# Optimization experiments

Measured on AMD Instinct MI355X. Metric: run time of the kernel, lower is better.

The kernel has to match this reference:

```python
import jax, jax.numpy as jnp
import numpy as np

N_NODES = 100000
N_EDGES = 1600000
N_GRAPHS = 1000
NODES_PER_GRAPH = N_NODES // N_GRAPHS
IN_DIM, HID_DIM, OUT_DIM = 32, 64, 32


def setup_inputs() -> dict:
    key = jax.random.key(0)
    k_x, k_src, k_dst, k_w1, k_w2 = jax.random.split(key, 5)
    x = jax.random.normal(k_x, (N_NODES, IN_DIM), dtype=jnp.float32)
    src = jax.random.randint(k_src, (N_EDGES,), 0, N_NODES, dtype=jnp.int32)
    dst = jax.random.randint(k_dst, (N_EDGES,), 0, N_NODES, dtype=jnp.int32)
    edge_index = jnp.stack([src, dst], axis=0)
    batch = (jnp.arange(N_NODES, dtype=jnp.int32) // NODES_PER_GRAPH)
    W1 = jax.random.normal(k_w1, (IN_DIM, HID_DIM), dtype=jnp.float32) / np.sqrt(IN_DIM)
    b1 = jnp.zeros((HID_DIM,), dtype=jnp.float32)
    W2 = jax.random.normal(k_w2, (HID_DIM, OUT_DIM), dtype=jnp.float32) / np.sqrt(HID_DIM)
    b2 = jnp.zeros((OUT_DIM,), dtype=jnp.float32)
    return {"x": x, "edge_index": edge_index, "batch": batch,
            "W1": W1, "b1": b1, "W2": W2, "b2": b2}


def _gcn_conv(x, W, b, src, dst, deg_inv_sqrt):
    # PyG GCNConv: out = D^{-1/2}(A+I)D^{-1/2} X W + b, deg includes self-loops
    h = x @ W  # [N, F]
    norm = deg_inv_sqrt[src] * deg_inv_sqrt[dst]  # [E]
    agg = jax.ops.segment_sum(h[src] * norm[:, None], dst, num_segments=N_NODES)
    # self-loop contribution: norm = deg^{-1/2} * deg^{-1/2} = 1/deg
    agg = agg + h * (deg_inv_sqrt * deg_inv_sqrt)[:, None]
    return agg + b


def reference(x, edge_index, batch, W1, b1, W2, b2):
    src, dst = edge_index[0], edge_index[1]
    # degree at target nodes, with self-loops
    deg = 1.0 + jax.ops.segment_sum(jnp.ones_like(dst, dtype=x.dtype), dst,
                                    num_segments=N_NODES)
    deg_inv_sqrt = jax.lax.rsqrt(deg)
    h = jax.nn.relu(_gcn_conv(x, W1, b1, src, dst, deg_inv_sqrt))
    h = _gcn_conv(h, W2, b2, src, dst, deg_inv_sqrt)
    # per-graph mean pooling (fused segment mean)
    sums = jax.ops.segment_sum(h, batch, num_segments=N_GRAPHS)
    counts = jax.ops.segment_sum(jnp.ones((h.shape[0],), dtype=h.dtype), batch,
                                 num_segments=N_GRAPHS)
    return sums / counts[:, None]
```

## Files before the change

kernel.cpp:

```cpp
#include <hip/hip_runtime.h>

#define IN_DIM 32
#define HID_DIM 64
#define OUT_DIM 32

#define BSHIFT 7
#define BNODES 128
#define BMASK 127
#define MAXBUCK 1024
#define CAP 2560
#define EPB 2048

typedef unsigned int u32;
typedef unsigned short u16;
typedef __attribute__((ext_vector_type(8))) short bf16x8;
typedef __attribute__((ext_vector_type(4))) float f32x4;

static __device__ __forceinline__ u32 bf16rne(float f) {
    u32 u = __float_as_uint(f);
    return (u + 0x7FFFu + ((u >> 16) & 1u)) >> 16;
}
static __device__ __forceinline__ float blo(u32 u) { return __uint_as_float(u << 16); }
static __device__ __forceinline__ float bhi(u32 u) { return __uint_as_float(u & 0xFFFF0000u); }

__global__ __launch_bounds__(256) void k_bin(const int* __restrict__ src,
                                             const int* __restrict__ dst,
                                             int* __restrict__ cursor,
                                             int* __restrict__ binned,
                                             int E, int nbuck) {
    __shared__ int lcnt[MAXBUCK];
    __shared__ int lbase[MAXBUCK];
    int t = threadIdx.x;
#pragma unroll
    for (int k = 0; k < MAXBUCK / 256; k++) lcnt[t + k * 256] = 0;
    __syncthreads();
    int base = blockIdx.x * EPB;
    int dreg[8];
#pragma unroll
    for (int k = 0; k < 8; k++) {
        int e = base + k * 256 + t;
        dreg[k] = (e < E) ? dst[e] : -1;
    }
#pragma unroll
    for (int k = 0; k < 8; k++)
        if (dreg[k] >= 0) atomicAdd(&lcnt[dreg[k] >> BSHIFT], 1);
    __syncthreads();
    for (int b = t; b < nbuck; b += 256) {
        int c = lcnt[b];
        if (c) lbase[b] = atomicAdd(&cursor[b], c);
        lcnt[b] = 0;
    }
    __syncthreads();
#pragma unroll
    for (int k = 0; k < 8; k++) {
        int e = base + k * 256 + t;
        if (dreg[k] >= 0) {
            int d = dreg[k];
            int bk = d >> BSHIFT;
            int loc = lbase[bk] + atomicAdd(&lcnt[bk], 1);
            if (loc < CAP)
                binned[bk * CAP + loc] = ((d & BMASK) << 17) | src[e];
        }
    }
}

__global__ __launch_bounds__(256) void k_csr(const int* __restrict__ binned,
                                             const int* __restrict__ cursor,
                                             const float* __restrict__ x,
                                             int2* __restrict__ row,
                                             float* __restrict__ dis,
                                             u16* __restrict__ g,
                                             int* __restrict__ meta, int N) {
    __shared__ int sEdge[CAP];
    __shared__ int sH[4][BNODES];
    __shared__ int sExcl[BNODES];
    __shared__ int sCur[BNODES];
    __shared__ float sdis[BNODES];
    __shared__ int wsum[2];
    int b = blockIdx.x;
    int t = threadIdx.x;
    int wid = t >> 6;
    int s0 = b * CAP;
    int cnt = cursor[b];
    if (cnt > CAP) cnt = CAP;

    for (int k = t; k < 4 * BNODES; k += 256) ((int*)sH)[k] = 0;
    __syncthreads();

    for (int k = t; k < cnt; k += 256) {
        int p = binned[s0 + k];
        sEdge[k] = p;
        atomicAdd(&sH[wid][p >> 17], 1);
    }
    __syncthreads();

    int myv = 0;
    if (t < BNODES) {
        myv = sH[0][t] + sH[1][t] + sH[2][t] + sH[3][t];
        int lane = t & 63;
        int incl = myv;
#pragma unroll
        for (int o = 1; o < 64; o <<= 1) {
            int up = __shfl_up(incl, o);
            if (lane >= o) incl += up;
        }
        if (lane == 63) wsum[t >> 6] = incl;
        sExcl[t] = incl - myv;
        sCur[t] = 0;
    }
    __syncthreads();
    if (t < BNODES) {
        int exclv = sExcl[t] + ((t >= 64) ? wsum[0] : 0);
        sExcl[t] = exclv;
        float d = rsqrtf(1.0f + (float)myv);
        sdis[t] = d;
        int node = (b << BSHIFT) + t;
        if (node < N) {
            row[node] = make_int2(s0 + exclv, s0 + exclv + myv);
            dis[node] = d;
        }
    }
    __syncthreads();

    for (int k = t; k < cnt; k += 256) {
        int p = sEdge[k];
        int dl = p >> 17;
        int pos = sExcl[dl] + atomicAdd(&sCur[dl], 1);
        meta[s0 + pos] = p & 0x1FFFF;
    }

    int nbLo = b << BSHIFT;
    int nn = N - nbLo;
    if (nn > BNODES) nn = BNODES;
    if (nn < 0) nn = 0;
    int halfE = nn * 16;
    const float* xb = x + (size_t)nbLo * 32;
    u32* gb = (u32*)(g + (size_t)nbLo * 32);
    for (int j = t; j < halfE; j += 256) {
        int e0 = j * 2;
        float dd = sdis[e0 >> 5];
        gb[j] = bf16rne(dd * xb[e0]) | (bf16rne(dd * xb[e0 + 1]) << 16);
    }
}

__global__ __launch_bounds__(256) void k_agg(const u16* __restrict__ g,
                                             const int* __restrict__ meta,
                                             const int2* __restrict__ row,
                                             const float* __restrict__ dis,
                                             u16* __restrict__ outf, int N) {
    int gid = blockIdx.x * 256 + threadIdx.x;
    int i = gid >> 5;
    if (i >= N) return;
    int l = threadIdx.x & 31;
    int grp = (l >> 2) & 7;
    int sub = l & 3;
    const uint4* gv = (const uint4*)g;

    float a0 = 0.f, a1 = 0.f, a2 = 0.f, a3 = 0.f;
    float a4 = 0.f, a5 = 0.f, a6 = 0.f, a7 = 0.f;
    int2 rw = row[i];
    int e = rw.x, end = rw.y;
    for (; e + 16 <= end; e += 16) {
        int s0 = meta[e + grp];
        int s1 = meta[e + 8 + grp];
        uint4 v0 = gv[s0 * 4 + sub];
        uint4 v1 = gv[s1 * 4 + sub];
        a0 += blo(v0.x); a1 += bhi(v0.x); a2 += blo(v0.y); a3 += bhi(v0.y);
        a4 += blo(v0.z); a5 += bhi(v0.z); a6 += blo(v0.w); a7 += bhi(v0.w);
        a0 += blo(v1.x); a1 += bhi(v1.x); a2 += blo(v1.y); a3 += bhi(v1.y);
        a4 += blo(v1.z); a5 += bhi(v1.z); a6 += blo(v1.w); a7 += bhi(v1.w);
    }
    if (e + grp < end) {
        uint4 v = gv[meta[e + grp] * 4 + sub];
        a0 += blo(v.x); a1 += bhi(v.x); a2 += blo(v.y); a3 += bhi(v.y);
        a4 += blo(v.z); a5 += bhi(v.z); a6 += blo(v.w); a7 += bhi(v.w);
    }
    if (e + 8 + grp < end) {
        uint4 v = gv[meta[e + 8 + grp] * 4 + sub];
        a0 += blo(v.x); a1 += bhi(v.x); a2 += blo(v.y); a3 += bhi(v.y);
        a4 += blo(v.z); a5 += bhi(v.z); a6 += blo(v.w); a7 += bhi(v.w);
    }
#pragma unroll
    for (int m = 4; m <= 16; m <<= 1) {
        a0 += __shfl_xor(a0, m); a1 += __shfl_xor(a1, m);
        a2 += __shfl_xor(a2, m); a3 += __shfl_xor(a3, m);
        a4 += __shfl_xor(a4, m); a5 += __shfl_xor(a5, m);
        a6 += __shfl_xor(a6, m); a7 += __shfl_xor(a7, m);
    }
    if (grp == 0) {
        uint4 sv = gv[i * 4 + sub];
        float d = dis[i];
        u32 o0 = bf16rne(d * (a0 + blo(sv.x))) | (bf16rne(d * (a1 + bhi(sv.x))) << 16);
        u32 o1 = bf16rne(d * (a2 + blo(sv.y))) | (bf16rne(d * (a3 + bhi(sv.y))) << 16);
        u32 o2 = bf16rne(d * (a4 + blo(sv.z))) | (bf16rne(d * (a5 + bhi(sv.z))) << 16);
        u32 o3 = bf16rne(d * (a6 + blo(sv.w))) | (bf16rne(d * (a7 + bhi(sv.w))) << 16);
        ((uint4*)outf)[i * 4 + sub] = make_uint4(o0, o1, o2, o3);
    }
}

__global__ __launch_bounds__(256) void k_mlp(const u16* __restrict__ aggX,
                                             const float* __restrict__ W1,
                                             const float* __restrict__ b1,
                                             const float* __restrict__ W2,
                                             const float* __restrict__ b2,
                                             const float* __restrict__ dis,
                                             u16* __restrict__ t2,
                                             float* __restrict__ out,
                                             int N, int outElems) {
    __shared__ float sHls[4][16 * 65];
    int t = threadIdx.x;
    int j = blockIdx.x * 256 + t;
    if (j < outElems) out[j] = b2[j & 31];

    int w = t >> 6;
    int L = t & 63;
    int q = L >> 4;
    int col = L & 15;
    int base = blockIdx.x * 64 + w * 16;

    int arow = base + col;
    uint4 av = (arow < N) ? ((const uint4*)aggX)[(size_t)arow * 4 + q]
                          : make_uint4(0, 0, 0, 0);
    bf16x8 afrag = *(bf16x8*)&av;

    bf16x8 b1f[4];
#pragma unroll
    for (int nt = 0; nt < 4; nt++) {
#pragma unroll
        for (int jj = 0; jj < 8; jj++)
            b1f[nt][jj] = (short)bf16rne(W1[(q * 8 + jj) * HID_DIM + nt * 16 + col]);
    }
    bf16x8 b2f[2][2];
#pragma unroll
    for (int ks = 0; ks < 2; ks++)
#pragma unroll
        for (int nt = 0; nt < 2; nt++) {
#pragma unroll
            for (int jj = 0; jj < 8; jj++)
                b2f[ks][nt][jj] =
                    (short)bf16rne(W2[(ks * 32 + q * 8 + jj) * OUT_DIM + nt * 16 + col]);
        }

    float bias = 0.0f;
#pragma unroll
    for (int nt = 0; nt < 4; nt++) {
        bias = b1[nt * 16 + col];
        f32x4 c = {bias, bias, bias, bias};
        c = __builtin_amdgcn_mfma_f32_16x16x32_bf16(afrag, b1f[nt], c, 0, 0, 0);
#pragma unroll
        for (int r = 0; r < 4; r++)
            sHls[w][(q * 4 + r) * 65 + nt * 16 + col] = fmaxf(c[r], 0.0f);
    }
    __syncthreads();

    bf16x8 a2[2];
#pragma unroll
    for (int ks = 0; ks < 2; ks++) {
#pragma unroll
        for (int jj = 0; jj < 8; jj++)
            a2[ks][jj] = (short)bf16rne(sHls[w][col * 65 + ks * 32 + q * 8 + jj]);
    }

    f32x4 C2[2];
#pragma unroll
    for (int nt = 0; nt < 2; nt++) {
        f32x4 c = {0.f, 0.f, 0.f, 0.f};
        c = __builtin_amdgcn_mfma_f32_16x16x32_bf16(a2[0], b2f[0][nt], c, 0, 0, 0);
        c = __builtin_amdgcn_mfma_f32_16x16x32_bf16(a2[1], b2f[1][nt], c, 0, 0, 0);
        C2[nt] = c;
    }

#pragma unroll
    for (int r = 0; r < 4; r++) {
        int node = base + q * 4 + r;
        if (node < N) {
            float dd = dis[node];
            t2[(size_t)node * 32 + col]      = (u16)bf16rne(dd * C2[0][r]);
            t2[(size_t)node * 32 + 16 + col] = (u16)bf16rne(dd * C2[1][r]);
        }
    }
}

__global__ __launch_bounds__(256) void k_agg_pool(const u16* __restrict__ g,
                                                  const int* __restrict__ meta,
                                                  const int2* __restrict__ row,
                                                  const float* __restrict__ dis,
                                                  float* __restrict__ out,
                                                  int N, int npg, float inv_npg) {
    __shared__ float sval[8][32];
    int t = threadIdx.x;
    int hw = t >> 5;
    int base0 = blockIdx.x * 8;
    int i = base0 + hw;
    int l = t & 31;
    int grp = (l >> 2) & 7;
    int sub = l & 3;
    const uint4* gv = (const uint4*)g;

    float a0 = 0.f, a1 = 0.f, a2 = 0.f, a3 = 0.f;
    float a4 = 0.f, a5 = 0.f, a6 = 0.f, a7 = 0.f;
    bool valid = (i < N);
    if (valid) {
        int2 rw = row[i];
        int e = rw.x, end = rw.y;
        for (; e + 16 <= end; e += 16) {
            int s0 = meta[e + grp];
            int s1 = meta[e + 8 + grp];
            uint4 v0 = gv[s0 * 4 + sub];
            uint4 v1 = gv[s1 * 4 + sub];
            a0 += blo(v0.x); a1 += bhi(v0.x); a2 += blo(v0.y); a3 += bhi(v0.y);
            a4 += blo(v0.z); a5 += bhi(v0.z); a6 += blo(v0.w); a7 += bhi(v0.w);
            a0 += blo(v1.x); a1 += bhi(v1.x); a2 += blo(v1.y); a3 += bhi(v1.y);
            a4 += blo(v1.z); a5 += bhi(v1.z); a6 += blo(v1.w); a7 += bhi(v1.w);
        }
        if (e + grp < end) {
            uint4 v = gv[meta[e + grp] * 4 + sub];
            a0 += blo(v.x); a1 += bhi(v.x); a2 += blo(v.y); a3 += bhi(v.y);
            a4 += blo(v.z); a5 += bhi(v.z); a6 += blo(v.w); a7 += bhi(v.w);
        }
        if (e + 8 + grp < end) {
            uint4 v = gv[meta[e + 8 + grp] * 4 + sub];
            a0 += blo(v.x); a1 += bhi(v.x); a2 += blo(v.y); a3 += bhi(v.y);
            a4 += blo(v.z); a5 += bhi(v.z); a6 += blo(v.w); a7 += bhi(v.w);
        }
    }
#pragma unroll
    for (int m = 4; m <= 16; m <<= 1) {
        a0 += __shfl_xor(a0, m); a1 += __shfl_xor(a1, m);
        a2 += __shfl_xor(a2, m); a3 += __shfl_xor(a3, m);
        a4 += __shfl_xor(a4, m); a5 += __shfl_xor(a5, m);
        a6 += __shfl_xor(a6, m); a7 += __shfl_xor(a7, m);
    }
    if (grp == 0) {
        float4 r0 = make_float4(0.f, 0.f, 0.f, 0.f);
        float4 r1 = make_float4(0.f, 0.f, 0.f, 0.f);
        if (valid) {
            uint4 sv = gv[i * 4 + sub];
            float d = dis[i];
            r0.x = d * (a0 + blo(sv.x)); r0.y = d * (a1 + bhi(sv.x));
            r0.z = d * (a2 + blo(sv.y)); r0.w = d * (a3 + bhi(sv.y));
            r1.x = d * (a4 + blo(sv.z)); r1.y = d * (a5 + bhi(sv.z));
            r1.z = d * (a6 + blo(sv.w)); r1.w = d * (a7 + bhi(sv.w));
        }
        float4* sp = (float4*)&sval[hw][0];
        sp[sub * 2 + 0] = r0;
        sp[sub * 2 + 1] = r1;
    }
    __syncthreads();
    if (t < 32) {
        int gfirst = base0 / npg;
        int bound = (gfirst + 1) * npg;
        float acc = 0.0f;
        int curg = gfirst;
#pragma unroll
        for (int h = 0; h < 8; h++) {
            int node = base0 + h;
            if (node >= N) break;
            int gg = (node >= bound) ? gfirst + 1 : gfirst;
            if (gg != curg) {
                atomicAdd(&out[curg * 32 + t], acc * inv_npg);
                acc = 0.0f;
                curg = gg;
            }
            acc += sval[h][t];
        }
        atomicAdd(&out[curg * 32 + t], acc * inv_npg);
    }
}

extern "C" void kernel_launch(void* const* d_in, const int* in_sizes, int n_in,
                              void* d_out, int out_size, void* d_ws, size_t ws_size,
                              hipStream_t stream) {
    const float* x   = (const float*)d_in[0];
    const int* eidx  = (const int*)d_in[1];
    const float* W1  = (const float*)d_in[3];
    const float* b1  = (const float*)d_in[4];
    const float* W2  = (const float*)d_in[5];
    const float* b2  = (const float*)d_in[6];
    float* out       = (float*)d_out;

    const int N = in_sizes[0] / IN_DIM;
    const int E = in_sizes[1] / 2;
    const int G = out_size / OUT_DIM;
    const int npg = N / G;
    const int nbuck = (N + BNODES - 1) >> BSHIFT;
    const int* src = eidx;
    const int* dst = eidx + E;

    char* ws = (char*)d_ws;
    size_t off = 0;
    auto alloc = [&](size_t bytes) -> char* {
        char* p = ws + off;
        off = (off + bytes + 255) & ~(size_t)255;
        return p;
    };
    int*   cursor = (int*)alloc(MAXBUCK * sizeof(int));
    int2*  row    = (int2*)alloc((size_t)N * sizeof(int2));
    float* dis    = (float*)alloc((size_t)N * sizeof(float));
    int*   binned = (int*)alloc((size_t)nbuck * CAP * sizeof(int));
    int*   meta   = (int*)alloc((size_t)nbuck * CAP * sizeof(int));
    u16*   g      = (u16*)alloc((size_t)N * IN_DIM * sizeof(u16));
    u16*   bufA   = (u16*)alloc((size_t)N * IN_DIM * sizeof(u16));
    u16*   bufB   = (u16*)alloc((size_t)N * OUT_DIM * sizeof(u16));
    (void)ws_size;

    hipMemsetAsync(cursor, 0, MAXBUCK * sizeof(int), stream);

    k_bin<<<(E + EPB - 1) / EPB, 256, 0, stream>>>(src, dst, cursor, binned, E, nbuck);
    k_csr<<<nbuck, 256, 0, stream>>>(binned, cursor, x, row, dis, g, meta, N);
    k_agg<<<((size_t)N * 32 + 255) / 256, 256, 0, stream>>>(g, meta, row, dis, bufA, N);
    k_mlp<<<(N + 63) / 64, 256, 0, stream>>>(bufA, W1, b1, W2, b2, dis, bufB, out,
                                             N, G * OUT_DIM);
    k_agg_pool<<<(N + 7) / 8, 256, 0, stream>>>(bufB, meta, row, dis, out,
                                                N, npg, 1.0f / (float)npg);
}
```

Before: 192.6 us.

## Widen binning buckets to 256 nodes and split CSR build across two blocks

The edge binning pass now uses 256-node buckets, halving the bucket count. This means fewer global cursor atomics per binning block and fewer, larger contiguous bins. The CSR-building kernel launches two blocks per bucket. Each block redundantly loads and histograms the whole bucket, then writes row/degree data, meta entries and scaled features only for its own 128-node half. The trade-off is duplicated loading and histogramming of bucket edges in exchange for coarser bins, and CAP per bucket doubles.

```diff
diff --git a/kernel.cpp b/kernel.cpp
--- a/kernel.cpp
+++ b/kernel.cpp
@@ -4,11 +4,10 @@
 #define HID_DIM 64
 #define OUT_DIM 32
 
-#define BSHIFT 7
-#define BNODES 128
-#define BMASK 127
-#define MAXBUCK 1024
-#define CAP 2560
+#define WSHIFT 8
+#define WMASK 255
+#define MAXBUCK 512
+#define CAP 5120
 #define EPB 2048
 
 typedef unsigned int u32;
@@ -31,8 +30,7 @@
     __shared__ int lcnt[MAXBUCK];
     __shared__ int lbase[MAXBUCK];
     int t = threadIdx.x;
-#pragma unroll
-    for (int k = 0; k < MAXBUCK / 256; k++) lcnt[t + k * 256] = 0;
+    lcnt[t] = 0; lcnt[t + 256] = 0;
     __syncthreads();
     int base = blockIdx.x * EPB;
     int dreg[8];
@@ -43,7 +41,7 @@
     }
 #pragma unroll
     for (int k = 0; k < 8; k++)
-        if (dreg[k] >= 0) atomicAdd(&lcnt[dreg[k] >> BSHIFT], 1);
+        if (dreg[k] >= 0) atomicAdd(&lcnt[dreg[k] >> WSHIFT], 1);
     __syncthreads();
     for (int b = t; b < nbuck; b += 256) {
         int c = lcnt[b];
@@ -56,10 +54,10 @@
         int e = base + k * 256 + t;
         if (dreg[k] >= 0) {
             int d = dreg[k];
-            int bk = d >> BSHIFT;
+            int bk = d >> WSHIFT;
             int loc = lbase[bk] + atomicAdd(&lcnt[bk], 1);
             if (loc < CAP)
-                binned[bk * CAP + loc] = ((d & BMASK) << 17) | src[e];
+                binned[bk * CAP + loc] = ((d & WMASK) << 17) | src[e];
         }
     }
 }
@@ -72,19 +70,21 @@
                                              u16* __restrict__ g,
                                              int* __restrict__ meta, int N) {
     __shared__ int sEdge[CAP];
-    __shared__ int sH[4][BNODES];
-    __shared__ int sExcl[BNODES];
-    __shared__ int sCur[BNODES];
-    __shared__ float sdis[BNODES];
-    __shared__ int wsum[2];
-    int b = blockIdx.x;
+    __shared__ int sH[4][256];
+    __shared__ int sExcl[256];
+    __shared__ int sCur[128];
+    __shared__ float sdis[128];
+    __shared__ int wsum[4];
+    int bb = blockIdx.x;
+    int b = bb >> 1;
+    int h = bb & 1;
     int t = threadIdx.x;
     int wid = t >> 6;
     int s0 = b * CAP;
     int cnt = cursor[b];
     if (cnt > CAP) cnt = CAP;
 
-    for (int k = t; k < 4 * BNODES; k += 256) ((int*)sH)[k] = 0;
+    for (int k = t; k < 4 * 256; k += 256) ((int*)sH)[k] = 0;
     __syncthreads();
 
     for (int k = t; k < cnt; k += 256) {
@@ -94,27 +94,29 @@
     }
     __syncthreads();
 
-    int myv = 0;
-    if (t < BNODES) {
-        myv = sH[0][t] + sH[1][t] + sH[2][t] + sH[3][t];
-        int lane = t & 63;
-        int incl = myv;
-#pragma unroll
-        for (int o = 1; o < 64; o <<= 1) {
-            int up = __shfl_up(incl, o);
-            if (lane >= o) incl += up;
-        }
-        if (lane == 63) wsum[t >> 6] = incl;
-        sExcl[t] = incl - myv;
-        sCur[t] = 0;
-    }
-    __syncthreads();
-    if (t < BNODES) {
-        int exclv = sExcl[t] + ((t >= 64) ? wsum[0] : 0);
-        sExcl[t] = exclv;
+    int myv = sH[0][t] + sH[1][t] + sH[2][t] + sH[3][t];
+    int lane = t & 63;
+    int incl = myv;
+#pragma unroll
+    for (int o = 1; o < 64; o <<= 1) {
+        int up = __shfl_up(incl, o);
+        if (lane >= o) incl += up;
+    }
+    if (lane == 63) wsum[wid] = incl;
+    sExcl[t] = incl - myv;
+    if (t < 128) sCur[t] = 0;
+    __syncthreads();
+    int wpre = 0;
+#pragma unroll
+    for (int w = 0; w < 4; w++) wpre += (w < wid) ? wsum[w] : 0;
+    int exclv = sExcl[t] + wpre;
+    sExcl[t] = exclv;
+
+    bool mine = ((t >> 7) == h);
+    if (mine) {
         float d = rsqrtf(1.0f + (float)myv);
-        sdis[t] = d;
-        int node = (b << BSHIFT) + t;
+        sdis[t & 127] = d;
+        int node = (b << WSHIFT) + t;
         if (node < N) {
             row[node] = make_int2(s0 + exclv, s0 + exclv + myv);
             dis[node] = d;
@@ -125,13 +127,15 @@
     for (int k = t; k < cnt; k += 256) {
         int p = sEdge[k];
         int dl = p >> 17;
-        int pos = sExcl[dl] + atomicAdd(&sCur[dl], 1);
-        meta[s0 + pos] = p & 0x1FFFF;
-    }
-
-    int nbLo = b << BSHIFT;
+        if ((dl >> 7) == h) {
+            int pos = sExcl[dl] + atomicAdd(&sCur[dl & 127], 1);
+            meta[s0 + pos] = p & 0x1FFFF;
+        }
+    }
+
+    int nbLo = (b << WSHIFT) + h * 128;
     int nn = N - nbLo;
-    if (nn > BNODES) nn = BNODES;
+    if (nn > 128) nn = 128;
     if (nn < 0) nn = 0;
     int halfE = nn * 16;
     const float* xb = x + (size_t)nbLo * 32;
@@ -241,10 +245,9 @@
                     (short)bf16rne(W2[(ks * 32 + q * 8 + jj) * OUT_DIM + nt * 16 + col]);
         }
 
-    float bias = 0.0f;
 #pragma unroll
     for (int nt = 0; nt < 4; nt++) {
-        bias = b1[nt * 16 + col];
+        float bias = b1[nt * 16 + col];
         f32x4 c = {bias, bias, bias, bias};
         c = __builtin_amdgcn_mfma_f32_16x16x32_bf16(afrag, b1f[nt], c, 0, 0, 0);
 #pragma unroll
@@ -383,7 +386,7 @@
     const int E = in_sizes[1] / 2;
     const int G = out_size / OUT_DIM;
     const int npg = N / G;
-    const int nbuck = (N + BNODES - 1) >> BSHIFT;
+    const int nbuck = (N + 255) >> WSHIFT;
     const int* src = eidx;
     const int* dst = eidx + E;
 
@@ -407,7 +410,7 @@
     hipMemsetAsync(cursor, 0, MAXBUCK * sizeof(int), stream);
 
     k_bin<<<(E + EPB - 1) / EPB, 256, 0, stream>>>(src, dst, cursor, binned, E, nbuck);
-    k_csr<<<nbuck, 256, 0, stream>>>(binned, cursor, x, row, dis, g, meta, N);
+    k_csr<<<2 * nbuck, 256, 0, stream>>>(binned, cursor, x, row, dis, g, meta, N);
     k_agg<<<((size_t)N * 32 + 255) / 256, 256, 0, stream>>>(g, meta, row, dis, bufA, N);
     k_mlp<<<(N + 63) / 64, 256, 0, stream>>>(bufA, W1, b1, W2, b2, dis, bufB, out,
                                              N, G * OUT_DIM);
```

After: 189.5 us. No clear change (-1.6%).

## Bucket edges by graph and pool second layer per graph without per-node aggregation

Applied to the files above, without the earlier changes.

Edges are now bucketed by graph (npg nodes per bucket, via magic-number division) instead of fixed 128-node buckets. The final layer-2 aggregation plus mean pooling is replaced by a per-graph kernel. Because pooling is linear, it sums dis[dst]*g[src] over the edges in each bucket plus the self terms directly, so per-node layer-2 outputs and global float atomics are never formed. This removes the CSR walk over all nodes in the last layer and moves bias initialisation into the pool kernel. In exchange, one 256-thread block handles each graph's roughly 1600 edges. The change also assumes npg is at most 128 and that nodes are contiguously batched.

```diff
diff --git a/kernel.cpp b/kernel.cpp
--- a/kernel.cpp
+++ b/kernel.cpp
@@ -4,15 +4,13 @@
 #define HID_DIM 64
 #define OUT_DIM 32
 
-#define BSHIFT 7
-#define BNODES 128
-#define BMASK 127
 #define MAXBUCK 1024
 #define CAP 2560
 #define EPB 2048
 
 typedef unsigned int u32;
 typedef unsigned short u16;
+typedef unsigned long long u64;
 typedef __attribute__((ext_vector_type(8))) short bf16x8;
 typedef __attribute__((ext_vector_type(4))) float f32x4;
 
@@ -27,7 +25,7 @@
                                              const int* __restrict__ dst,
                                              int* __restrict__ cursor,
                                              int* __restrict__ binned,
-                                             int E, int nbuck) {
+                                             int E, int nbuck, int npg, u32 M) {
     __shared__ int lcnt[MAXBUCK];
     __shared__ int lbase[MAXBUCK];
     int t = threadIdx.x;
@@ -35,15 +33,19 @@
     for (int k = 0; k < MAXBUCK / 256; k++) lcnt[t + k * 256] = 0;
     __syncthreads();
     int base = blockIdx.x * EPB;
-    int dreg[8];
+    int dreg[8], breg[8];
 #pragma unroll
     for (int k = 0; k < 8; k++) {
         int e = base + k * 256 + t;
         dreg[k] = (e < E) ? dst[e] : -1;
     }
 #pragma unroll
-    for (int k = 0; k < 8; k++)
-        if (dreg[k] >= 0) atomicAdd(&lcnt[dreg[k] >> BSHIFT], 1);
+    for (int k = 0; k < 8; k++) {
+        if (dreg[k] >= 0) {
+            breg[k] = (int)(((u64)(u32)dreg[k] * M) >> 38);
+            atomicAdd(&lcnt[breg[k]], 1);
+        }
+    }
     __syncthreads();
     for (int b = t; b < nbuck; b += 256) {
         int c = lcnt[b];
@@ -53,13 +55,12 @@
     __syncthreads();
 #pragma unroll
     for (int k = 0; k < 8; k++) {
-        int e = base + k * 256 + t;
         if (dreg[k] >= 0) {
-            int d = dreg[k];
-            int bk = d >> BSHIFT;
+            int bk = breg[k];
+            int dl = dreg[k] - bk * npg;
             int loc = lbase[bk] + atomicAdd(&lcnt[bk], 1);
             if (loc < CAP)
-                binned[bk * CAP + loc] = ((d & BMASK) << 17) | src[e];
+                binned[bk * CAP + loc] = (dl << 17) | src[base + k * 256 + t];
         }
     }
 }
@@ -70,12 +71,13 @@
                                              int2* __restrict__ row,
                                              float* __restrict__ dis,
                                              u16* __restrict__ g,
-                                             int* __restrict__ meta, int N) {
+                                             int* __restrict__ meta,
+                                             int N, int npg) {
     __shared__ int sEdge[CAP];
-    __shared__ int sH[4][BNODES];
-    __shared__ int sExcl[BNODES];
-    __shared__ int sCur[BNODES];
-    __shared__ float sdis[BNODES];
+    __shared__ int sH[4][128];
+    __shared__ int sExcl[128];
+    __shared__ int sCur[128];
+    __shared__ float sdis[128];
     __shared__ int wsum[2];
     int b = blockIdx.x;
     int t = threadIdx.x;
@@ -84,7 +86,7 @@
     int cnt = cursor[b];
     if (cnt > CAP) cnt = CAP;
 
-    for (int k = t; k < 4 * BNODES; k += 256) ((int*)sH)[k] = 0;
+    for (int k = t; k < 4 * 128; k += 256) ((int*)sH)[k] = 0;
     __syncthreads();
 
     for (int k = t; k < cnt; k += 256) {
@@ -94,9 +96,8 @@
     }
     __syncthreads();
 
-    int myv = 0;
-    if (t < BNODES) {
-        myv = sH[0][t] + sH[1][t] + sH[2][t] + sH[3][t];
+    if (t < 128) {
+        int myv = sH[0][t] + sH[1][t] + sH[2][t] + sH[3][t];
         int lane = t & 63;
         int incl = myv;
 #pragma unroll
@@ -107,15 +108,17 @@
         if (lane == 63) wsum[t >> 6] = incl;
         sExcl[t] = incl - myv;
         sCur[t] = 0;
-    }
-    __syncthreads();
-    if (t < BNODES) {
+        sH[0][t] = myv;
+    }
+    __syncthreads();
+    if (t < 128) {
         int exclv = sExcl[t] + ((t >= 64) ? wsum[0] : 0);
         sExcl[t] = exclv;
+        int myv = sH[0][t];
         float d = rsqrtf(1.0f + (float)myv);
         sdis[t] = d;
-        int node = (b << BSHIFT) + t;
-        if (node < N) {
+        int node = b * npg + t;
+        if (t < npg && node < N) {
             row[node] = make_int2(s0 + exclv, s0 + exclv + myv);
             dis[node] = d;
         }
@@ -129,9 +132,9 @@
         meta[s0 + pos] = p & 0x1FFFF;
     }
 
-    int nbLo = b << BSHIFT;
+    int nbLo = b * npg;
     int nn = N - nbLo;
-    if (nn > BNODES) nn = BNODES;
+    if (nn > npg) nn = npg;
     if (nn < 0) nn = 0;
     int halfE = nn * 16;
     const float* xb = x + (size_t)nbLo * 32;
@@ -202,16 +205,10 @@
                                              const float* __restrict__ W1,
                                              const float* __restrict__ b1,
                                              const float* __restrict__ W2,
-                                             const float* __restrict__ b2,
                                              const float* __restrict__ dis,
-                                             u16* __restrict__ t2,
-                                             float* __restrict__ out,
-                                             int N, int outElems) {
+                                             u16* __restrict__ t2, int N) {
     __shared__ float sHls[4][16 * 65];
     int t = threadIdx.x;
-    int j = blockIdx.x * 256 + t;
-    if (j < outElems) out[j] = b2[j & 31];
-
     int w = t >> 6;
     int L = t & 63;
     int q = L >> 4;
@@ -241,10 +238,9 @@
                     (short)bf16rne(W2[(ks * 32 + q * 8 + jj) * OUT_DIM + nt * 16 + col]);
         }
 
-    float bias = 0.0f;
 #pragma unroll
     for (int nt = 0; nt < 4; nt++) {
-        bias = b1[nt * 16 + col];
+        float bias = b1[nt * 16 + col];
         f32x4 c = {bias, bias, bias, bias};
         c = __builtin_amdgcn_mfma_f32_16x16x32_bf16(afrag, b1f[nt], c, 0, 0, 0);
 #pragma unroll
@@ -281,91 +277,87 @@
     }
 }
 
-__global__ __launch_bounds__(256) void k_agg_pool(const u16* __restrict__ g,
-                                                  const int* __restrict__ meta,
-                                                  const int2* __restrict__ row,
-                                                  const float* __restrict__ dis,
-                                                  float* __restrict__ out,
-                                                  int N, int npg, float inv_npg) {
-    __shared__ float sval[8][32];
+__global__ __launch_bounds__(256) void k_pool2(const int* __restrict__ binned,
+                                               const int* __restrict__ cursor,
+                                               const u16* __restrict__ gB,
+                                               const float* __restrict__ dis,
+                                               const float* __restrict__ b2,
+                                               float* __restrict__ out,
+                                               int N, int npg, float inv_npg) {
+    __shared__ float sdis[128];
+    __shared__ float sacc[32];
+    int b = blockIdx.x;
     int t = threadIdx.x;
-    int hw = t >> 5;
-    int base0 = blockIdx.x * 8;
-    int i = base0 + hw;
-    int l = t & 31;
-    int grp = (l >> 2) & 7;
-    int sub = l & 3;
-    const uint4* gv = (const uint4*)g;
+    if (t < 128) {
+        int node = b * npg + t;
+        sdis[t] = (t < npg && node < N) ? dis[node] : 0.0f;
+    }
+    if (t < 32) sacc[t] = 0.0f;
+    __syncthreads();
+
+    int s0 = b * CAP;
+    int cnt = cursor[b];
+    if (cnt > CAP) cnt = CAP;
+    int sub = t & 3;
+    int et = t >> 2;
+    const uint4* gv = (const uint4*)gB;
 
     float a0 = 0.f, a1 = 0.f, a2 = 0.f, a3 = 0.f;
     float a4 = 0.f, a5 = 0.f, a6 = 0.f, a7 = 0.f;
-    bool valid = (i < N);
-    if (valid) {
-        int2 rw = row[i];
-        int e = rw.x, end = rw.y;
-        for (; e + 16 <= end; e += 16) {
-            int s0 = meta[e + grp];
-            int s1 = meta[e + 8 + grp];
-            uint4 v0 = gv[s0 * 4 + sub];
-            uint4 v1 = gv[s1 * 4 + sub];
-            a0 += blo(v0.x); a1 += bhi(v0.x); a2 += blo(v0.y); a3 += bhi(v0.y);
-            a4 += blo(v0.z); a5 += bhi(v0.z); a6 += blo(v0.w); a7 += bhi(v0.w);
-            a0 += blo(v1.x); a1 += bhi(v1.x); a2 += blo(v1.y); a3 += bhi(v1.y);
-            a4 += blo(v1.z); a5 += bhi(v1.z); a6 += blo(v1.w); a7 += bhi(v1.w);
-        }
-        if (e + grp < end) {
-            uint4 v = gv[meta[e + grp] * 4 + sub];
-            a0 += blo(v.x); a1 += bhi(v.x); a2 += blo(v.y); a3 += bhi(v.y);
-            a4 += blo(v.z); a5 += bhi(v.z); a6 += blo(v.w); a7 += bhi(v.w);
-        }
-        if (e + 8 + grp < end) {
-            uint4 v = gv[meta[e + 8 + grp] * 4 + sub];
-            a0 += blo(v.x); a1 += bhi(v.x); a2 += blo(v.y); a3 += bhi(v.y);
-            a4 += blo(v.z); a5 += bhi(v.z); a6 += blo(v.w); a7 += bhi(v.w);
-        }
-    }
-#pragma unroll
-    for (int m = 4; m <= 16; m <<= 1) {
+    int e = et;
+    int p0 = 0;
+    uint4 v0 = make_uint4(0, 0, 0, 0);
+    bool have = (e < cnt);
+    if (have) { p0 = binned[s0 + e]; v0 = gv[(p0 & 0x1FFFF) * 4 + sub]; }
+    for (; e + 64 < cnt; e += 64) {
+        int p1 = binned[s0 + e + 64];
+        uint4 v1 = gv[(p1 & 0x1FFFF) * 4 + sub];
+        float w = sdis[p0 >> 17];
+        a0 = fmaf(w, blo(v0.x), a0); a1 = fmaf(w, bhi(v0.x), a1);
+        a2 = fmaf(w, blo(v0.y), a2); a3 = fmaf(w, bhi(v0.y), a3);
+        a4 = fmaf(w, blo(v0.z), a4); a5 = fmaf(w, bhi(v0.z), a5);
+        a6 = fmaf(w, blo(v0.w), a6); a7 = fmaf(w, bhi(v0.w), a7);
+        p0 = p1; v0 = v1;
+    }
+    if (have) {
+        float w = sdis[p0 >> 17];
+        a0 = fmaf(w, blo(v0.x), a0); a1 = fmaf(w, bhi(v0.x), a1);
+        a2 = fmaf(w, blo(v0.y), a2); a3 = fmaf(w, bhi(v0.y), a3);
+        a4 = fmaf(w, blo(v0.z), a4); a5 = fmaf(w, bhi(v0.z), a5);
+        a6 = fmaf(w, blo(v0.w), a6); a7 = fmaf(w, bhi(v0.w), a7);
+    }
+#pragma unroll
+    for (int m = 4; m <= 32; m <<= 1) {
         a0 += __shfl_xor(a0, m); a1 += __shfl_xor(a1, m);
         a2 += __shfl_xor(a2, m); a3 += __shfl_xor(a3, m);
         a4 += __shfl_xor(a4, m); a5 += __shfl_xor(a5, m);
         a6 += __shfl_xor(a6, m); a7 += __shfl_xor(a7, m);
     }
-    if (grp == 0) {
-        float4 r0 = make_float4(0.f, 0.f, 0.f, 0.f);
-        float4 r1 = make_float4(0.f, 0.f, 0.f, 0.f);
-        if (valid) {
-            uint4 sv = gv[i * 4 + sub];
-            float d = dis[i];
-            r0.x = d * (a0 + blo(sv.x)); r0.y = d * (a1 + bhi(sv.x));
-            r0.z = d * (a2 + blo(sv.y)); r0.w = d * (a3 + bhi(sv.y));
-            r1.x = d * (a4 + blo(sv.z)); r1.y = d * (a5 + bhi(sv.z));
-            r1.z = d * (a6 + blo(sv.w)); r1.w = d * (a7 + bhi(sv.w));
-        }
-        float4* sp = (float4*)&sval[hw][0];
-        sp[sub * 2 + 0] = r0;
-        sp[sub * 2 + 1] = r1;
-    }
-    __syncthreads();
-    if (t < 32) {
-        int gfirst = base0 / npg;
-        int bound = (gfirst + 1) * npg;
-        float acc = 0.0f;
-        int curg = gfirst;
-#pragma unroll
-        for (int h = 0; h < 8; h++) {
-            int node = base0 + h;
-            if (node >= N) break;
-            int gg = (node >= bound) ? gfirst + 1 : gfirst;
-            if (gg != curg) {
-                atomicAdd(&out[curg * 32 + t], acc * inv_npg);
-                acc = 0.0f;
-                curg = gg;
-            }
-            acc += sval[h][t];
-        }
-        atomicAdd(&out[curg * 32 + t], acc * inv_npg);
-    }
+    if ((t & 63) < 4) {
+        atomicAdd(&sacc[sub * 8 + 0], a0);
+        atomicAdd(&sacc[sub * 8 + 1], a1);
+        atomicAdd(&sacc[sub * 8 + 2], a2);
+        atomicAdd(&sacc[sub * 8 + 3], a3);
+        atomicAdd(&sacc[sub * 8 + 4], a4);
+        atomicAdd(&sacc[sub * 8 + 5], a5);
+        atomicAdd(&sacc[sub * 8 + 6], a6);
+        atomicAdd(&sacc[sub * 8 + 7], a7);
+    }
+
+    float accs = 0.0f;
+    int elems = npg * 32;
+    const u16* gbase = gB + (size_t)b * npg * 32;
+    int nbLo = b * npg;
+    for (int k = t; k < elems; k += 256) {
+        int node = k >> 5;
+        if (nbLo + node < N)
+            accs = fmaf(sdis[node], __uint_as_float((u32)gbase[k] << 16), accs);
+    }
+    atomicAdd(&sacc[t & 31], accs);
+    __syncthreads();
+
+    if (t < 32)
+        out[b * 32 + t] = fmaf(sacc[t], inv_npg, b2[t]);
 }
 
 extern "C" void kernel_launch(void* const* d_in, const int* in_sizes, int n_in,
@@ -383,9 +375,10 @@
     const int E = in_sizes[1] / 2;
     const int G = out_size / OUT_DIM;
     const int npg = N / G;
-    const int nbuck = (N + BNODES - 1) >> BSHIFT;
+    const int nbuck = G;
     const int* src = eidx;
     const int* dst = eidx + E;
+    const u32 M = (u32)(((1ull << 38) + npg - 1) / (u64)npg);
 
     char* ws = (char*)d_ws;
     size_t off = 0;
@@ -406,11 +399,11 @@
 
     hipMemsetAsync(cursor, 0, MAXBUCK * sizeof(int), stream);
 
-    k_bin<<<(E + EPB - 1) / EPB, 256, 0, stream>>>(src, dst, cursor, binned, E, nbuck);
-    k_csr<<<nbuck, 256, 0, stream>>>(binned, cursor, x, row, dis, g, meta, N);
+    k_bin<<<(E + EPB - 1) / EPB, 256, 0, stream>>>(src, dst, cursor, binned,
+                                                   E, nbuck, npg, M);
+    k_csr<<<nbuck, 256, 0, stream>>>(binned, cursor, x, row, dis, g, meta, N, npg);
     k_agg<<<((size_t)N * 32 + 255) / 256, 256, 0, stream>>>(g, meta, row, dis, bufA, N);
-    k_mlp<<<(N + 63) / 64, 256, 0, stream>>>(bufA, W1, b1, W2, b2, dis, bufB, out,
-                                             N, G * OUT_DIM);
-    k_agg_pool<<<(N + 7) / 8, 256, 0, stream>>>(bufB, meta, row, dis, out,
-                                                N, npg, 1.0f / (float)npg);
-}
+    k_mlp<<<(N + 63) / 64, 256, 0, stream>>>(bufA, W1, b1, W2, dis, bufB, N);
+    k_pool2<<<nbuck, 256, 0, stream>>>(binned, cursor, bufB, dis, b2, out,
+                                       N, npg, 1.0f / (float)npg);
+}
```

Measured after the change: 183.6 us. 4.7% less time.
